# Performance work log

Measured on AMD Instinct MI355X. Metric: run time of the kernel, lower is better.

## Reference

```python
import jax, jax.numpy as jnp
import numpy as np

N_NODES = 100000
N_EDGES = 1600000
IN_FEATS = 128
HID = 128
OUT_FEATS = 64


def setup_inputs() -> dict:
    key = jax.random.key(0)
    ks = jax.random.split(key, 8)
    node_ids = jnp.arange(N_NODES, dtype=jnp.int64)
    src = jax.random.randint(ks[0], (N_EDGES,), 0, N_NODES, dtype=jnp.int64)
    dst = jax.random.randint(ks[1], (N_EDGES,), 0, N_NODES, dtype=jnp.int64)
    emb = jax.random.normal(ks[2], (N_NODES, IN_FEATS), dtype=jnp.float32)
    W1 = jax.random.normal(ks[3], (IN_FEATS, HID), dtype=jnp.float32) / np.sqrt(IN_FEATS)
    b1 = jnp.zeros((HID,), dtype=jnp.float32)
    W2 = jax.random.normal(ks[4], (HID, OUT_FEATS), dtype=jnp.float32) / np.sqrt(HID)
    b2 = jnp.zeros((OUT_FEATS,), dtype=jnp.float32)
    return {"node_ids": node_ids, "src": src, "dst": dst, "emb": emb,
            "W1": W1, "b1": b1, "W2": W2, "b2": b2}


def _sym_norms(src, dst):
    # DGL GraphConv norm='both': D_out^{-1/2} on source side, D_in^{-1/2} on dest side,
    # degrees clamped to >= 1.
    ones = jnp.ones(src.shape[0], dtype=jnp.float32)
    deg_out = jax.ops.segment_sum(ones, src, num_segments=N_NODES)
    deg_in = jax.ops.segment_sum(ones, dst, num_segments=N_NODES)
    norm_src = jnp.clip(deg_out, 1.0, None) ** -0.5  # [N]
    norm_dst = jnp.clip(deg_in, 1.0, None) ** -0.5   # [N]
    return norm_src, norm_dst


def _spmm(src, dst, h):
    # rst[dst] += h[src]  (sparse adjacency aggregation)
    return jax.ops.segment_sum(h[src], dst, num_segments=N_NODES)


def reference(node_ids, src, dst, emb, W1, b1, W2, b2):
    norm_src, norm_dst = _sym_norms(src, dst)
    h = emb[node_ids]                                   # [N, IN]
    # Layer 1 (IN -> HID, relu): weight applied after aggregation (in <= out)
    h = _spmm(src, dst, h * norm_src[:, None]) * norm_dst[:, None]
    h = jax.nn.relu(h @ W1 + b1)                        # [N, HID]
    # Dropout(0.5) is identity in eval mode.
    # Layer 2 (HID -> OUT): DGL applies weight BEFORE aggregation when in > out
    h = (h @ W2) * norm_src[:, None]                    # [N, OUT]
    h = _spmm(src, dst, h) * norm_dst[:, None] + b2
    return h
```

## Files before the change

### kernel.cpp

```cpp
#include <hip/hip_runtime.h>

#define N_N 100000
#define N_E 1600000
#define SLOTS 48
#define N_PAD 100096

#define BK_SHIFT 9
#define BK_SIZE 512
#define NBKT 196
#define MAXB 10240
#define EPB2 4096
#define NBLK2 ((N_E + EPB2 - 1) / EPB2)

typedef unsigned short ushort_t;
typedef unsigned int uint_t;
typedef __bf16 bf16x8 __attribute__((ext_vector_type(8)));
typedef float f32x4 __attribute__((ext_vector_type(4)));

__device__ __forceinline__ ushort_t f2bf(float f) {
    uint_t u = __float_as_uint(f);
    u += 0x7fffu + ((u >> 16) & 1u);
    return (ushort_t)(u >> 16);
}

__device__ __forceinline__ uint_t pack_hl(float x) {
    uint_t xb = __float_as_uint(x);
    uint_t hb = (xb + 0x7fffu + ((xb >> 16) & 1u)) & 0xffff0000u;
    float rem = x - __uint_as_float(hb);
    uint_t rb = __float_as_uint(rem);
    uint_t lo = (rb + 0x7fffu + ((rb >> 16) & 1u)) >> 16;
    return (hb >> 16) | (lo << 16);
}

__device__ __forceinline__ bf16x8 as_bf16x8(uint4 u) {
    union { uint4 u; bf16x8 v; } c; c.u = u; return c.v;
}

__device__ __forceinline__ void unpack_frag(uint4 p0, uint4 p1, bf16x8& hi, bf16x8& lo) {
    uint4 h, l;
    h.x = (p0.x & 0xffffu) | (p0.y << 16);
    h.y = (p0.z & 0xffffu) | (p0.w << 16);
    h.z = (p1.x & 0xffffu) | (p1.y << 16);
    h.w = (p1.z & 0xffffu) | (p1.w << 16);
    l.x = (p0.x >> 16) | (p0.y & 0xffff0000u);
    l.y = (p0.z >> 16) | (p0.w & 0xffff0000u);
    l.z = (p1.x >> 16) | (p1.y & 0xffff0000u);
    l.w = (p1.z >> 16) | (p1.w & 0xffff0000u);
    hi = as_bf16x8(h); lo = as_bf16x8(l);
}

__global__ void __launch_bounds__(256) k_prep_pack(
        const float* __restrict__ emb, ushort_t* __restrict__ embb,
        const float* __restrict__ W1, const float* __restrict__ W2,
        uint_t* __restrict__ w1pk, uint_t* __restrict__ w2pk) {
    int b = blockIdx.x, t = threadIdx.x;
    if (b < 12500) {
        int i = b * 256 + t;
        float4 v = ((const float4*)emb)[i];
        ushort4 o;
        o.x = f2bf(v.x); o.y = f2bf(v.y); o.z = f2bf(v.z); o.w = f2bf(v.w);
        ((ushort4*)embb)[i] = o;
    } else {
        int idx = (b - 12500) * 256 + t;
        int j = idx & 7, l = (idx >> 3) & 63;
        int k = (l >> 4) * 8 + j;
        int n = l & 15;
        if (idx < 16384) {
            int kc = (idx >> 9) & 3, nt = idx >> 11;
            w1pk[idx] = pack_hl(W1[(kc * 32 + k) * 128 + nt * 16 + n]);
        } else {
            int i2 = idx - 16384;
            int kc = (i2 >> 9) & 3, nt = i2 >> 11;
            w2pk[i2] = pack_hl(W2[(kc * 32 + k) * 64 + nt * 16 + n]);
        }
    }
}

__global__ void __launch_bounds__(256) k_scatter(
        const int* __restrict__ src, const int* __restrict__ dst,
        int* __restrict__ cur_d, int* __restrict__ cur_s,
        uint2* __restrict__ pe_dst, int* __restrict__ pe_src) {
    __shared__ int hd[NBKT], hs[NBKT], od[NBKT], os_[NBKT];
    int t = threadIdx.x, blk = blockIdx.x;
    for (int i = t; i < NBKT; i += 256) { hd[i] = 0; hs[i] = 0; }
    __syncthreads();
    int e0 = blk * EPB2;
    int eend = min(e0 + EPB2, N_E);
    for (int e = e0 + t; e < eend; e += 256) {
        atomicAdd(&hd[dst[e] >> BK_SHIFT], 1);
        atomicAdd(&hs[src[e] >> BK_SHIFT], 1);
    }
    __syncthreads();
    for (int i = t; i < NBKT; i += 256) {
        int c = hd[i]; od[i]  = c ? atomicAdd(&cur_d[i], c) : 0;
        c = hs[i];     os_[i] = c ? atomicAdd(&cur_s[i], c) : 0;
    }
    __syncthreads();
    for (int i = t; i < NBKT; i += 256) { hd[i] = 0; hs[i] = 0; }
    __syncthreads();
    for (int e = e0 + t; e < eend; e += 256) {
        int s = src[e], d = dst[e];
        int bd = d >> BK_SHIFT, bs = s >> BK_SHIFT;
        int rd = od[bd]  + atomicAdd(&hd[bd], 1);
        int rs = os_[bs] + atomicAdd(&hs[bs], 1);
        if (rd < MAXB) pe_dst[(size_t)bd * MAXB + rd] = make_uint2((uint_t)s, (uint_t)d);
        if (rs < MAXB) pe_src[(size_t)bs * MAXB + rs] = s;
    }
}

__global__ void __launch_bounds__(512) k_binC(
        const uint2* __restrict__ pe_dst, const int* __restrict__ pe_src,
        const int* __restrict__ cur_d, const int* __restrict__ cur_s,
        int* __restrict__ slots, int* __restrict__ cnt,
        float* __restrict__ nd, float* __restrict__ ns) {
    __shared__ int lc[BK_SIZE];
    int t = threadIdx.x, bb = blockIdx.x;
    for (int i = t; i < BK_SIZE; i += 512) lc[i] = 0;
    __syncthreads();
    if (bb < NBKT) {
        int b = bb;
        int cb = min(cur_d[b], MAXB);
        int nbase = b << BK_SHIFT;
        const uint2* pe = pe_dst + (size_t)b * MAXB;
        for (int e = t; e < cb; e += 512) {
            uint2 ed = pe[e];
            int pos = atomicAdd(&lc[(int)ed.y - nbase], 1);
            if (pos < SLOTS) slots[(size_t)ed.y * SLOTS + pos] = (int)ed.x;
        }
        __syncthreads();
        for (int i = t; i < BK_SIZE; i += 512) {
            int n = nbase + i;
            if (n < N_N) {
                int c = lc[i];
                cnt[n] = c;
                nd[n] = 1.0f / sqrtf((float)max(c, 1));
            }
        }
    } else {
        int b = bb - NBKT;
        int cb = min(cur_s[b], MAXB);
        int nbase = b << BK_SHIFT;
        const int* pe = pe_src + (size_t)b * MAXB;
        for (int e = t; e < cb; e += 512)
            atomicAdd(&lc[pe[e] - nbase], 1);
        __syncthreads();
        for (int i = t; i < BK_SIZE; i += 512) {
            int n = nbase + i;
            if (n < N_N) ns[n] = 1.0f / sqrtf((float)max(lc[i], 1));
        }
    }
}

__global__ void __launch_bounds__(256) k_spmm1(
        const int* __restrict__ cnt, const int* __restrict__ slots,
        const ushort_t* __restrict__ embb, const float* __restrict__ ns,
        const float* __restrict__ nd, uint_t* __restrict__ aggpk) {
    int wid = (blockIdx.x * 256 + (int)threadIdx.x) >> 6;
    int node = __builtin_amdgcn_readfirstlane(wid);
    if (node >= N_N) return;
    int lane = threadIdx.x & 63;
    const int* row = slots + node * SLOTS;
    int len = min(cnt[node], SLOTS);
    float ax0 = 0.f, ay0 = 0.f, ax1 = 0.f, ay1 = 0.f;
    int e = 0;
    int n8 = len & ~7;
    for (; e < n8; e += 8) {
        int s0 = __builtin_amdgcn_readfirstlane(row[e + 0]);
        int s1 = __builtin_amdgcn_readfirstlane(row[e + 1]);
        int s2 = __builtin_amdgcn_readfirstlane(row[e + 2]);
        int s3 = __builtin_amdgcn_readfirstlane(row[e + 3]);
        int s4 = __builtin_amdgcn_readfirstlane(row[e + 4]);
        int s5 = __builtin_amdgcn_readfirstlane(row[e + 5]);
        int s6 = __builtin_amdgcn_readfirstlane(row[e + 6]);
        int s7 = __builtin_amdgcn_readfirstlane(row[e + 7]);
        float w0 = ns[s0], w1 = ns[s1], w2 = ns[s2], w3 = ns[s3];
        float w4 = ns[s4], w5 = ns[s5], w6 = ns[s6], w7 = ns[s7];
        uint_t v0 = ((const uint_t*)(embb + (size_t)s0 * 128))[lane];
        uint_t v1 = ((const uint_t*)(embb + (size_t)s1 * 128))[lane];
        uint_t v2 = ((const uint_t*)(embb + (size_t)s2 * 128))[lane];
        uint_t v3 = ((const uint_t*)(embb + (size_t)s3 * 128))[lane];
        uint_t v4 = ((const uint_t*)(embb + (size_t)s4 * 128))[lane];
        uint_t v5 = ((const uint_t*)(embb + (size_t)s5 * 128))[lane];
        uint_t v6 = ((const uint_t*)(embb + (size_t)s6 * 128))[lane];
        uint_t v7 = ((const uint_t*)(embb + (size_t)s7 * 128))[lane];
        ax0 = fmaf(__uint_as_float(v0 << 16), w0, ax0);
        ay0 = fmaf(__uint_as_float(v0 & 0xffff0000u), w0, ay0);
        ax1 = fmaf(__uint_as_float(v1 << 16), w1, ax1);
        ay1 = fmaf(__uint_as_float(v1 & 0xffff0000u), w1, ay1);
        ax0 = fmaf(__uint_as_float(v2 << 16), w2, ax0);
        ay0 = fmaf(__uint_as_float(v2 & 0xffff0000u), w2, ay0);
        ax1 = fmaf(__uint_as_float(v3 << 16), w3, ax1);
        ay1 = fmaf(__uint_as_float(v3 & 0xffff0000u), w3, ay1);
        ax0 = fmaf(__uint_as_float(v4 << 16), w4, ax0);
        ay0 = fmaf(__uint_as_float(v4 & 0xffff0000u), w4, ay0);
        ax1 = fmaf(__uint_as_float(v5 << 16), w5, ax1);
        ay1 = fmaf(__uint_as_float(v5 & 0xffff0000u), w5, ay1);
        ax0 = fmaf(__uint_as_float(v6 << 16), w6, ax0);
        ay0 = fmaf(__uint_as_float(v6 & 0xffff0000u), w6, ay0);
        ax1 = fmaf(__uint_as_float(v7 << 16), w7, ax1);
        ay1 = fmaf(__uint_as_float(v7 & 0xffff0000u), w7, ay1);
    }
    int n4 = len & ~3;
    for (; e < n4; e += 4) {
        int s0 = __builtin_amdgcn_readfirstlane(row[e + 0]);
        int s1 = __builtin_amdgcn_readfirstlane(row[e + 1]);
        int s2 = __builtin_amdgcn_readfirstlane(row[e + 2]);
        int s3 = __builtin_amdgcn_readfirstlane(row[e + 3]);
        float w0 = ns[s0], w1 = ns[s1], w2 = ns[s2], w3 = ns[s3];
        uint_t v0 = ((const uint_t*)(embb + (size_t)s0 * 128))[lane];
        uint_t v1 = ((const uint_t*)(embb + (size_t)s1 * 128))[lane];
        uint_t v2 = ((const uint_t*)(embb + (size_t)s2 * 128))[lane];
        uint_t v3 = ((const uint_t*)(embb + (size_t)s3 * 128))[lane];
        ax0 = fmaf(__uint_as_float(v0 << 16), w0, ax0);
        ay0 = fmaf(__uint_as_float(v0 & 0xffff0000u), w0, ay0);
        ax1 = fmaf(__uint_as_float(v1 << 16), w1, ax1);
        ay1 = fmaf(__uint_as_float(v1 & 0xffff0000u), w1, ay1);
        ax0 = fmaf(__uint_as_float(v2 << 16), w2, ax0);
        ay0 = fmaf(__uint_as_float(v2 & 0xffff0000u), w2, ay0);
        ax1 = fmaf(__uint_as_float(v3 << 16), w3, ax1);
        ay1 = fmaf(__uint_as_float(v3 & 0xffff0000u), w3, ay1);
    }
    for (; e < len; ++e) {
        int s = __builtin_amdgcn_readfirstlane(row[e]);
        float w = ns[s];
        uint_t v = ((const uint_t*)(embb + (size_t)s * 128))[lane];
        ax0 = fmaf(__uint_as_float(v << 16), w, ax0);
        ay0 = fmaf(__uint_as_float(v & 0xffff0000u), w, ay0);
    }
    float sc = nd[node];
    uint2 o;
    o.x = pack_hl((ax0 + ax1) * sc);
    o.y = pack_hl((ay0 + ay1) * sc);
    ((uint2*)(aggpk + (size_t)node * 128))[lane] = o;
}

#define HST 140
__global__ void __launch_bounds__(256) k_gemm(
        const uint_t* __restrict__ aggpk, const uint_t* __restrict__ w1pk,
        const float* __restrict__ b1, const uint_t* __restrict__ w2pk,
        const float* __restrict__ ns, ushort_t* __restrict__ h2b) {
    __shared__ uint_t sh[64 * HST];
    int t = threadIdx.x;
    int w = t >> 6, l = t & 63;
    int quad = l >> 4, lm = l & 15;
    int nb0 = blockIdx.x * 64;

    f32x4 acc[8];
#pragma unroll
    for (int i = 0; i < 8; i++) acc[i] = (f32x4){0.f, 0.f, 0.f, 0.f};
    const uint_t* abase = aggpk + (size_t)(nb0 + w * 16 + lm) * 128 + quad * 8;
    bf16x8 ahi[4], alo[4];
#pragma unroll
    for (int kc = 0; kc < 4; kc++) {
        uint4 p0 = *(const uint4*)(abase + kc * 32);
        uint4 p1 = *(const uint4*)(abase + kc * 32 + 4);
        unpack_frag(p0, p1, ahi[kc], alo[kc]);
    }
#pragma unroll
    for (int nt = 0; nt < 8; nt++) {
#pragma unroll
        for (int kc = 0; kc < 4; kc++) {
            const uint_t* bb = w1pk + (((nt * 4 + kc) * 64 + l) << 3);
            uint4 q0 = *(const uint4*)(bb);
            uint4 q1 = *(const uint4*)(bb + 4);
            bf16x8 bhi, blo;
            unpack_frag(q0, q1, bhi, blo);
            acc[nt] = __builtin_amdgcn_mfma_f32_16x16x32_bf16(ahi[kc], bhi, acc[nt], 0, 0, 0);
            acc[nt] = __builtin_amdgcn_mfma_f32_16x16x32_bf16(ahi[kc], blo, acc[nt], 0, 0, 0);
            acc[nt] = __builtin_amdgcn_mfma_f32_16x16x32_bf16(alo[kc], bhi, acc[nt], 0, 0, 0);
        }
    }
#pragma unroll
    for (int nt = 0; nt < 8; nt++) {
        float bb = b1[nt * 16 + lm];
#pragma unroll
        for (int r = 0; r < 4; r++) {
            int row = w * 16 + quad * 4 + r;
            float hv = fmaxf(acc[nt][r] + bb, 0.f);
            sh[row * HST + nt * 16 + lm] = pack_hl(hv);
        }
    }
    __syncthreads();

    f32x4 acc2[4];
#pragma unroll
    for (int i = 0; i < 4; i++) acc2[i] = (f32x4){0.f, 0.f, 0.f, 0.f};
    const uint_t* sbase = sh + (w * 16 + lm) * HST + quad * 8;
    bf16x8 hhi[4], hlo[4];
#pragma unroll
    for (int kc = 0; kc < 4; kc++) {
        uint4 p0 = *(const uint4*)(sbase + kc * 32);
        uint4 p1 = *(const uint4*)(sbase + kc * 32 + 4);
        unpack_frag(p0, p1, hhi[kc], hlo[kc]);
    }
#pragma unroll
    for (int nt = 0; nt < 4; nt++) {
#pragma unroll
        for (int kc = 0; kc < 4; kc++) {
            const uint_t* bb = w2pk + (((nt * 4 + kc) * 64 + l) << 3);
            uint4 q0 = *(const uint4*)(bb);
            uint4 q1 = *(const uint4*)(bb + 4);
            bf16x8 bhi, blo;
            unpack_frag(q0, q1, bhi, blo);
            acc2[nt] = __builtin_amdgcn_mfma_f32_16x16x32_bf16(hhi[kc], bhi, acc2[nt], 0, 0, 0);
            acc2[nt] = __builtin_amdgcn_mfma_f32_16x16x32_bf16(hhi[kc], blo, acc2[nt], 0, 0, 0);
            acc2[nt] = __builtin_amdgcn_mfma_f32_16x16x32_bf16(hlo[kc], bhi, acc2[nt], 0, 0, 0);
        }
    }
#pragma unroll
    for (int r = 0; r < 4; r++) {
        int node = nb0 + w * 16 + quad * 4 + r;
        if (node < N_N) {
            float s = ns[node];
#pragma unroll
            for (int nt = 0; nt < 4; nt++)
                h2b[(size_t)node * 64 + nt * 16 + lm] = f2bf(acc2[nt][r] * s);
        }
    }
}

__global__ void __launch_bounds__(256) k_spmm2(
        const int* __restrict__ cnt, const int* __restrict__ slots,
        const ushort_t* __restrict__ h2b, const float* __restrict__ nd,
        const float* __restrict__ b2, float* __restrict__ out) {
    int wid = (blockIdx.x * 256 + (int)threadIdx.x) >> 6;
    int node = __builtin_amdgcn_readfirstlane(wid);
    if (node >= N_N) return;
    int lane = threadIdx.x & 63;
    int half = lane >> 5, w32 = lane & 31;
    const int* row = slots + node * SLOTS;
    int len = min(cnt[node], SLOTS);
    const uint_t* H = (const uint_t*)h2b;
    float a0 = 0.f, a1 = 0.f, b0 = 0.f, b1v = 0.f;
    int e = 0;
    int n8 = len & ~7;
    for (; e < n8; e += 8) {
        int i0 = e + half;
        int s0 = row[i0], s1 = row[i0 + 2], s2 = row[i0 + 4], s3 = row[i0 + 6];
        uint_t v0 = H[(size_t)s0 * 32 + w32];
        uint_t v1 = H[(size_t)s1 * 32 + w32];
        uint_t v2 = H[(size_t)s2 * 32 + w32];
        uint_t v3 = H[(size_t)s3 * 32 + w32];
        a0 += __uint_as_float(v0 << 16); a1 += __uint_as_float(v0 & 0xffff0000u);
        b0 += __uint_as_float(v1 << 16); b1v += __uint_as_float(v1 & 0xffff0000u);
        a0 += __uint_as_float(v2 << 16); a1 += __uint_as_float(v2 & 0xffff0000u);
        b0 += __uint_as_float(v3 << 16); b1v += __uint_as_float(v3 & 0xffff0000u);
    }
    for (; e + 1 < len; e += 2) {
        int s = row[e + half];
        uint_t v = H[(size_t)s * 32 + w32];
        a0 += __uint_as_float(v << 16); a1 += __uint_as_float(v & 0xffff0000u);
    }
    if (e < len && half == 0) {
        int s = row[e];
        uint_t v = H[(size_t)s * 32 + w32];
        a0 += __uint_as_float(v << 16); a1 += __uint_as_float(v & 0xffff0000u);
    }
    a0 += b0; a1 += b1v;
    a0 += __shfl_xor(a0, 32);
    a1 += __shfl_xor(a1, 32);
    if (half == 0) {
        float sc = nd[node];
        float2 bb = ((const float2*)b2)[w32];
        float2 o;
        o.x = a0 * sc + bb.x;
        o.y = a1 * sc + bb.y;
        ((float2*)(out + (size_t)node * 64))[w32] = o;
    }
}

extern "C" void kernel_launch(void* const* d_in, const int* in_sizes, int n_in,
                              void* d_out, int out_size, void* d_ws, size_t ws_size,
                              hipStream_t stream) {
    const int* src = (const int*)d_in[1];
    const int* dst = (const int*)d_in[2];
    const float* emb = (const float*)d_in[3];
    const float* W1 = (const float*)d_in[4];
    const float* b1 = (const float*)d_in[5];
    const float* W2 = (const float*)d_in[6];
    const float* b2 = (const float*)d_in[7];
    float* out = (float*)d_out;

    int* cur_d   = (int*)d_ws;
    int* cur_s   = cur_d + 256;
    int* cnt     = cur_s + 256;
    float* ns    = (float*)(cnt + N_PAD);
    float* nd    = ns + N_PAD;
    int* slots   = (int*)(nd + N_PAD);
    uint2* pe_dst= (uint2*)(slots + (size_t)N_N * SLOTS);
    int* pe_src  = (int*)(pe_dst + (size_t)NBKT * MAXB);
    ushort_t* embb = (ushort_t*)(pe_src + (size_t)NBKT * MAXB);
    uint_t* aggpk = (uint_t*)(embb + (size_t)N_PAD * 128);
    uint_t* w1pk = aggpk + (size_t)N_PAD * 128;
    uint_t* w2pk = w1pk + 16384;
    ushort_t* h2b = (ushort_t*)(w2pk + 8192);

    hipMemsetAsync(cur_d, 0, sizeof(int) * 512, stream);
    k_prep_pack<<<12596, 256, 0, stream>>>(emb, embb, W1, W2, w1pk, w2pk);
    k_scatter  <<<NBLK2, 256, 0, stream>>>(src, dst, cur_d, cur_s, pe_dst, pe_src);
    k_binC     <<<2 * NBKT, 512, 0, stream>>>(pe_dst, pe_src, cur_d, cur_s, slots, cnt, nd, ns);
    k_spmm1    <<<(N_N + 3) / 4, 256, 0, stream>>>(cnt, slots, embb, ns, nd, aggpk);
    k_gemm     <<<(N_N + 63) / 64, 256, 0, stream>>>(aggpk, w1pk, b1, w2pk, ns, h2b);
    k_spmm2    <<<(N_N + 3) / 4, 256, 0, stream>>>(cnt, slots, h2b, nd, b2, out);
}
```

Measured before the change: 332.4 us.

## Fuse scatter with prep-pack kernel and compress dst-bucket edge records

Merges the edge bucket-scatter kernel and the embedding/weight bf16 packing kernel into one launch, with the scatter blocks placed first. This removes one kernel launch and lets the two independent phases overlap on the GPU. Each dst-bucket edge record shrinks from a uint2 pair to one 32-bit word holding the 17-bit source and the 9-bit local destination, which halves scatter write and binning read traffic. It also quadruples edges per scatter block, so there are fewer global atomics per bucket but less parallelism in that phase.

```diff
diff --git a/kernel.cpp b/kernel.cpp
--- a/kernel.cpp
+++ b/kernel.cpp
@@ -9,8 +9,10 @@
 #define BK_SIZE 512
 #define NBKT 196
 #define MAXB 10240
-#define EPB2 4096
+#define EPB2 16384
 #define NBLK2 ((N_E + EPB2 - 1) / EPB2)
+#define NBLK_EMB 12500
+#define NBLK_W 96
 
 typedef unsigned short ushort_t;
 typedef unsigned int uint_t;
@@ -49,42 +51,42 @@
     hi = as_bf16x8(h); lo = as_bf16x8(l);
 }
 
-__global__ void __launch_bounds__(256) k_prep_pack(
+__global__ void __launch_bounds__(256) k_scatter_prep(
+        const int* __restrict__ src, const int* __restrict__ dst,
+        int* __restrict__ cur_d, int* __restrict__ cur_s,
+        uint_t* __restrict__ pe_dst, uint_t* __restrict__ pe_src,
         const float* __restrict__ emb, ushort_t* __restrict__ embb,
         const float* __restrict__ W1, const float* __restrict__ W2,
         uint_t* __restrict__ w1pk, uint_t* __restrict__ w2pk) {
     int b = blockIdx.x, t = threadIdx.x;
-    if (b < 12500) {
-        int i = b * 256 + t;
-        float4 v = ((const float4*)emb)[i];
-        ushort4 o;
-        o.x = f2bf(v.x); o.y = f2bf(v.y); o.z = f2bf(v.z); o.w = f2bf(v.w);
-        ((ushort4*)embb)[i] = o;
-    } else {
-        int idx = (b - 12500) * 256 + t;
-        int j = idx & 7, l = (idx >> 3) & 63;
-        int k = (l >> 4) * 8 + j;
-        int n = l & 15;
-        if (idx < 16384) {
-            int kc = (idx >> 9) & 3, nt = idx >> 11;
-            w1pk[idx] = pack_hl(W1[(kc * 32 + k) * 128 + nt * 16 + n]);
+    if (b >= NBLK2) {
+        int pb = b - NBLK2;
+        if (pb < NBLK_EMB) {
+            int i = pb * 256 + t;
+            float4 v = ((const float4*)emb)[i];
+            ushort4 o;
+            o.x = f2bf(v.x); o.y = f2bf(v.y); o.z = f2bf(v.z); o.w = f2bf(v.w);
+            ((ushort4*)embb)[i] = o;
         } else {
-            int i2 = idx - 16384;
-            int kc = (i2 >> 9) & 3, nt = i2 >> 11;
-            w2pk[i2] = pack_hl(W2[(kc * 32 + k) * 64 + nt * 16 + n]);
-        }
-    }
-}
-
-__global__ void __launch_bounds__(256) k_scatter(
-        const int* __restrict__ src, const int* __restrict__ dst,
-        int* __restrict__ cur_d, int* __restrict__ cur_s,
-        uint2* __restrict__ pe_dst, int* __restrict__ pe_src) {
+            int idx = (pb - NBLK_EMB) * 256 + t;
+            int j = idx & 7, l = (idx >> 3) & 63;
+            int k = (l >> 4) * 8 + j;
+            int n = l & 15;
+            if (idx < 16384) {
+                int kc = (idx >> 9) & 3, nt = idx >> 11;
+                w1pk[idx] = pack_hl(W1[(kc * 32 + k) * 128 + nt * 16 + n]);
+            } else {
+                int i2 = idx - 16384;
+                int kc = (i2 >> 9) & 3, nt = i2 >> 11;
+                w2pk[i2] = pack_hl(W2[(kc * 32 + k) * 64 + nt * 16 + n]);
+            }
+        }
+        return;
+    }
     __shared__ int hd[NBKT], hs[NBKT], od[NBKT], os_[NBKT];
-    int t = threadIdx.x, blk = blockIdx.x;
     for (int i = t; i < NBKT; i += 256) { hd[i] = 0; hs[i] = 0; }
     __syncthreads();
-    int e0 = blk * EPB2;
+    int e0 = b * EPB2;
     int eend = min(e0 + EPB2, N_E);
     for (int e = e0 + t; e < eend; e += 256) {
         atomicAdd(&hd[dst[e] >> BK_SHIFT], 1);
@@ -103,13 +105,13 @@
         int bd = d >> BK_SHIFT, bs = s >> BK_SHIFT;
         int rd = od[bd]  + atomicAdd(&hd[bd], 1);
         int rs = os_[bs] + atomicAdd(&hs[bs], 1);
-        if (rd < MAXB) pe_dst[(size_t)bd * MAXB + rd] = make_uint2((uint_t)s, (uint_t)d);
-        if (rs < MAXB) pe_src[(size_t)bs * MAXB + rs] = s;
+        if (rd < MAXB) pe_dst[(size_t)bd * MAXB + rd] = (uint_t)s | ((uint_t)(d & 511) << 17);
+        if (rs < MAXB) pe_src[(size_t)bs * MAXB + rs] = (uint_t)s;
     }
 }
 
 __global__ void __launch_bounds__(512) k_binC(
-        const uint2* __restrict__ pe_dst, const int* __restrict__ pe_src,
+        const uint_t* __restrict__ pe_dst, const uint_t* __restrict__ pe_src,
         const int* __restrict__ cur_d, const int* __restrict__ cur_s,
         int* __restrict__ slots, int* __restrict__ cnt,
         float* __restrict__ nd, float* __restrict__ ns) {
@@ -121,11 +123,13 @@
         int b = bb;
         int cb = min(cur_d[b], MAXB);
         int nbase = b << BK_SHIFT;
-        const uint2* pe = pe_dst + (size_t)b * MAXB;
+        const uint_t* pe = pe_dst + (size_t)b * MAXB;
         for (int e = t; e < cb; e += 512) {
-            uint2 ed = pe[e];
-            int pos = atomicAdd(&lc[(int)ed.y - nbase], 1);
-            if (pos < SLOTS) slots[(size_t)ed.y * SLOTS + pos] = (int)ed.x;
+            uint_t ed = pe[e];
+            int dloc = (int)(ed >> 17);
+            int s = (int)(ed & 0x1ffffu);
+            int pos = atomicAdd(&lc[dloc], 1);
+            if (pos < SLOTS) slots[(size_t)(nbase + dloc) * SLOTS + pos] = s;
         }
         __syncthreads();
         for (int i = t; i < BK_SIZE; i += 512) {
@@ -140,9 +144,9 @@
         int b = bb - NBKT;
         int cb = min(cur_s[b], MAXB);
         int nbase = b << BK_SHIFT;
-        const int* pe = pe_src + (size_t)b * MAXB;
+        const uint_t* pe = pe_src + (size_t)b * MAXB;
         for (int e = t; e < cb; e += 512)
-            atomicAdd(&lc[pe[e] - nbase], 1);
+            atomicAdd(&lc[(int)pe[e] - nbase], 1);
         __syncthreads();
         for (int i = t; i < BK_SIZE; i += 512) {
             int n = nbase + i;
@@ -387,8 +391,8 @@
     float* ns    = (float*)(cnt + N_PAD);
     float* nd    = ns + N_PAD;
     int* slots   = (int*)(nd + N_PAD);
-    uint2* pe_dst= (uint2*)(slots + (size_t)N_N * SLOTS);
-    int* pe_src  = (int*)(pe_dst + (size_t)NBKT * MAXB);
+    uint_t* pe_dst = (uint_t*)(slots + (size_t)N_N * SLOTS);
+    uint_t* pe_src = pe_dst + (size_t)NBKT * MAXB;
     ushort_t* embb = (ushort_t*)(pe_src + (size_t)NBKT * MAXB);
     uint_t* aggpk = (uint_t*)(embb + (size_t)N_PAD * 128);
     uint_t* w1pk = aggpk + (size_t)N_PAD * 128;
@@ -396,10 +400,10 @@
     ushort_t* h2b = (ushort_t*)(w2pk + 8192);
 
     hipMemsetAsync(cur_d, 0, sizeof(int) * 512, stream);
-    k_prep_pack<<<12596, 256, 0, stream>>>(emb, embb, W1, W2, w1pk, w2pk);
-    k_scatter  <<<NBLK2, 256, 0, stream>>>(src, dst, cur_d, cur_s, pe_dst, pe_src);
-    k_binC     <<<2 * NBKT, 512, 0, stream>>>(pe_dst, pe_src, cur_d, cur_s, slots, cnt, nd, ns);
-    k_spmm1    <<<(N_N + 3) / 4, 256, 0, stream>>>(cnt, slots, embb, ns, nd, aggpk);
-    k_gemm     <<<(N_N + 63) / 64, 256, 0, stream>>>(aggpk, w1pk, b1, w2pk, ns, h2b);
-    k_spmm2    <<<(N_N + 3) / 4, 256, 0, stream>>>(cnt, slots, h2b, nd, b2, out);
-}
+    k_scatter_prep<<<NBLK2 + NBLK_EMB + NBLK_W, 256, 0, stream>>>(
+        src, dst, cur_d, cur_s, pe_dst, pe_src, emb, embb, W1, W2, w1pk, w2pk);
+    k_binC  <<<2 * NBKT, 512, 0, stream>>>(pe_dst, pe_src, cur_d, cur_s, slots, cnt, nd, ns);
+    k_spmm1 <<<(N_N + 3) / 4, 256, 0, stream>>>(cnt, slots, embb, ns, nd, aggpk);
+    k_gemm  <<<(N_N + 63) / 64, 256, 0, stream>>>(aggpk, w1pk, b1, w2pk, ns, h2b);
+    k_spmm2 <<<(N_N + 3) / 4, 256, 0, stream>>>(cnt, slots, h2b, nd, b2, out);
+}
```

New measurement: 369.3 us. 11.1% more time.
